# Performance work log

Measured on AMD Instinct MI355X. Metric: run time of the kernel, lower is better.

## Reference

```python
import jax, jax.numpy as jnp
import numpy as np

VOCAB = 32000


def setup_inputs() -> dict:
    key = jax.random.key(0)
    k1, k2, k3, k4, k5 = jax.random.split(key, 5)
    B, H, DEC_T, ATTN_LEN, D = 16, 12, 128, 512, 768
    return {
        "dec_output": jax.random.normal(k1, (B, DEC_T, D), dtype=jnp.float32),
        "final_output": jax.random.normal(k2, (B, DEC_T, VOCAB), dtype=jnp.float32),
        "attention_weights": jax.random.normal(k3, (B, H, DEC_T, ATTN_LEN), dtype=jnp.float32),
        "encoder_input": jax.random.randint(k4, (B, ATTN_LEN), 0, VOCAB, dtype=jnp.int32),
        "W_pg": jax.random.normal(k5, (D, 1), dtype=jnp.float32) / np.sqrt(D),
        "b_pg": jnp.zeros((1,), dtype=jnp.float32),
    }


def reference(dec_output, final_output, attention_weights, encoder_input, W_pg, b_pg):
    # p_gen: Dense(1) + sigmoid  -> [B, dec_t, 1]
    p_gen = jax.nn.sigmoid(dec_output @ W_pg + b_pg)

    vocab_dist = jax.nn.softmax(final_output, axis=-1)          # [B, dec_t, V]

    # mean_attention_heads=True: average over the heads axis
    attn_mean = jnp.mean(attention_weights, axis=1)              # [B, dec_t, attn_len]
    attn_dist = jax.nn.softmax(attn_mean, axis=-1)

    vocab_dists = p_gen * vocab_dist
    attn_dists = (1.0 - p_gen) * attn_dist

    dec_t = attn_dist.shape[1]

    # Per-example scatter-add of attention mass onto vocab ids.
    # For each batch b: proj[t, encoder_input[b, j]] += attn_dists[b, t, j]
    def scatter_one(ids, a):  # ids: [attn_len] int, a: [dec_t, attn_len]
        return jnp.zeros((dec_t, VOCAB), dtype=a.dtype).at[:, ids].add(a)

    attn_dists_projected = jax.vmap(scatter_one)(encoder_input, attn_dists)

    final_dists = attn_dists_projected + vocab_dists
    return jnp.log(final_dists)
```

## Files before the change

### kernel.cpp

```cpp
#include <hip/hip_runtime.h>
#include <math.h>

#define VOCAB 32000
#define NB 16
#define NH 12
#define DEC_T 128
#define ALEN 512
#define DD 768
#define NT 1024
#define NW 16
#define V4 8000
#define CHUNKS 8

__device__ inline float wave_sum(float v) {
#pragma unroll
  for (int o = 32; o > 0; o >>= 1) v += __shfl_down(v, o, 64);
  return v;
}
__device__ inline float wave_max(float v) {
#pragma unroll
  for (int o = 32; o > 0; o >>= 1) v = fmaxf(v, __shfl_down(v, o, 64));
  return v;
}

__global__ __launch_bounds__(NT, 4) void pg_kernel(
    const float* __restrict__ dec, const float* __restrict__ fo,
    const float* __restrict__ attnw, const int* __restrict__ ids,
    const float* __restrict__ Wpg, const float* __restrict__ bpg,
    float* __restrict__ out) {
  __shared__ float s_vocab[VOCAB];
  __shared__ float s_red[NW];
  __shared__ float s_res[8];

  const int bt = blockIdx.x;
  const int b = bt / DEC_T;
  const int t = bt - b * DEC_T;
  const int tid = threadIdx.x;
  const int lane = tid & 63;
  const int wid = tid >> 6;

  const float4* row4 = (const float4*)(fo + (size_t)bt * VOCAB);
  float4 r[CHUNKS];
#pragma unroll
  for (int c = 0; c < CHUNKS; ++c) {
    int idx = c * NT + tid;
    if (idx < V4) r[c] = row4[idx];
  }

  for (int i = tid; i < VOCAB; i += NT) s_vocab[i] = 0.f;

  float pp = 0.f;
  if (tid < DD) pp = dec[(size_t)bt * DD + tid] * Wpg[tid];
  pp = wave_sum(pp);
  if (lane == 0) s_red[wid] = pp;
  __syncthreads();
  if (tid == 0) {
    float acc = 0.f;
    for (int i = 0; i < NW; ++i) acc += s_red[i];
    s_res[0] = acc;
  }
  __syncthreads();
  const float pgen = 1.f / (1.f + __expf(-(s_res[0] + bpg[0])));

  float amean = 0.f;
  float av = -INFINITY;
  if (tid < ALEN) {
    const float* ap = attnw + ((size_t)b * NH * DEC_T + t) * ALEN + tid;
    float s = 0.f;
#pragma unroll
    for (int h = 0; h < NH; ++h) s += ap[(size_t)h * DEC_T * ALEN];
    amean = s * (1.f / NH);
    av = amean;
  }
  float am = wave_max(av);
  if (lane == 0) s_red[wid] = am;
  __syncthreads();
  if (tid == 0) {
    float acc = -INFINITY;
    for (int i = 0; i < NW; ++i) acc = fmaxf(acc, s_red[i]);
    s_res[1] = acc;
  }
  __syncthreads();
  const float amax = s_res[1];
  float ae = (tid < ALEN) ? __expf(amean - amax) : 0.f;
  float as = wave_sum(ae);
  if (lane == 0) s_red[wid] = as;
  __syncthreads();
  if (tid == 0) {
    float acc = 0.f;
    for (int i = 0; i < NW; ++i) acc += s_red[i];
    s_res[2] = acc;
  }
  __syncthreads();
  const float ainv = (1.f - pgen) / s_res[2];
  if (tid < ALEN) atomicAdd(&s_vocab[ids[b * ALEN + tid]], ae * ainv);

  float m = -INFINITY;
#pragma unroll
  for (int c = 0; c < CHUNKS; ++c) {
    int idx = c * NT + tid;
    if (idx < V4)
      m = fmaxf(m, fmaxf(fmaxf(r[c].x, r[c].y), fmaxf(r[c].z, r[c].w)));
  }
  m = wave_max(m);
  if (lane == 0) s_red[wid] = m;
  __syncthreads();
  if (tid == 0) {
    float acc = -INFINITY;
    for (int i = 0; i < NW; ++i) acc = fmaxf(acc, s_red[i]);
    s_res[3] = acc;
  }
  __syncthreads();
  const float fm = s_res[3];

  float zs = 0.f;
#pragma unroll
  for (int c = 0; c < CHUNKS; ++c) {
    int idx = c * NT + tid;
    if (idx < V4)
      zs += __expf(r[c].x - fm) + __expf(r[c].y - fm) +
            __expf(r[c].z - fm) + __expf(r[c].w - fm);
  }
  zs = wave_sum(zs);
  if (lane == 0) s_red[wid] = zs;
  __syncthreads();
  if (tid == 0) {
    float acc = 0.f;
    for (int i = 0; i < NW; ++i) acc += s_red[i];
    s_res[4] = acc;
  }
  __syncthreads();
  const float Z = s_res[4];
  const float invZ = 1.f / Z;
  const float C = __logf(pgen) - fm - __logf(Z);

  float4* out4 = (float4*)(out + (size_t)bt * VOCAB);
#pragma unroll
  for (int c = 0; c < CHUNKS; ++c) {
    int idx = c * NT + tid;
    if (idx < V4) {
      const int v = idx * 4;
      const float4 x = r[c];
      const float s0 = s_vocab[v + 0];
      const float s1 = s_vocab[v + 1];
      const float s2 = s_vocab[v + 2];
      const float s3 = s_vocab[v + 3];
      float4 o;
      o.x = (s0 == 0.f) ? (x.x + C) : __logf(pgen * __expf(x.x - fm) * invZ + s0);
      o.y = (s1 == 0.f) ? (x.y + C) : __logf(pgen * __expf(x.y - fm) * invZ + s1);
      o.z = (s2 == 0.f) ? (x.z + C) : __logf(pgen * __expf(x.z - fm) * invZ + s2);
      o.w = (s3 == 0.f) ? (x.w + C) : __logf(pgen * __expf(x.w - fm) * invZ + s3);
      out4[idx] = o;
    }
  }
}

extern "C" void kernel_launch(void* const* d_in, const int* in_sizes, int n_in,
                              void* d_out, int out_size, void* d_ws, size_t ws_size,
                              hipStream_t stream) {
  (void)in_sizes; (void)n_in; (void)out_size; (void)d_ws; (void)ws_size;
  const float* dec   = (const float*)d_in[0];
  const float* fo    = (const float*)d_in[1];
  const float* attnw = (const float*)d_in[2];
  const int*   ids   = (const int*)  d_in[3];
  const float* Wpg   = (const float*)d_in[4];
  const float* bpg   = (const float*)d_in[5];
  float* out = (float*)d_out;

  pg_kernel<<<NB * DEC_T, NT, 0, stream>>>(dec, fo, attnw, ids, Wpg, bpg, out);
}
```

Baseline: 481.3 us.

## Replace dense vocab LDS array with hash table plus bitmap, halve block size

Result: slower. 513.9 us (+6.8%).

```diff
diff --git a/kernel.cpp b/kernel.cpp
--- a/kernel.cpp
+++ b/kernel.cpp
@@ -7,10 +7,14 @@
 #define DEC_T 128
 #define ALEN 512
 #define DD 768
-#define NT 1024
-#define NW 16
+#define NT 512
+#define NW 8
 #define V4 8000
-#define CHUNKS 8
+#define CHUNKS 16
+#define HSZ 1024
+#define BMW 1000
+
+typedef float f4 __attribute__((ext_vector_type(4)));
 
 __device__ inline float wave_sum(float v) {
 #pragma unroll
@@ -28,9 +32,11 @@
     const float* __restrict__ attnw, const int* __restrict__ ids,
     const float* __restrict__ Wpg, const float* __restrict__ bpg,
     float* __restrict__ out) {
-  __shared__ float s_vocab[VOCAB];
-  __shared__ float s_red[NW];
-  __shared__ float s_res[8];
+  __shared__ int      h_key[HSZ];
+  __shared__ float    h_val[HSZ];
+  __shared__ unsigned bm[BMW];
+  __shared__ float    s_red[NW];
+  __shared__ float    s_res[8];
 
   const int bt = blockIdx.x;
   const int b = bt / DEC_T;
@@ -39,18 +45,27 @@
   const int lane = tid & 63;
   const int wid = tid >> 6;
 
-  const float4* row4 = (const float4*)(fo + (size_t)bt * VOCAB);
-  float4 r[CHUNKS];
+  const f4* row4 = (const f4*)(fo + (size_t)bt * VOCAB);
+  f4 r[CHUNKS];
 #pragma unroll
   for (int c = 0; c < CHUNKS; ++c) {
     int idx = c * NT + tid;
-    if (idx < V4) r[c] = row4[idx];
+    if (idx < V4) {
+      r[c] = row4[idx];
+    } else {
+      f4 z = {0.f, 0.f, 0.f, 0.f};
+      r[c] = z;
+    }
   }
+#pragma unroll
+  for (int c = 0; c < CHUNKS; ++c) asm volatile("" : "+v"(r[c]));
 
-  for (int i = tid; i < VOCAB; i += NT) s_vocab[i] = 0.f;
+  for (int i = tid; i < HSZ; i += NT) { h_key[i] = -1; h_val[i] = 0.f; }
+  for (int i = tid; i < BMW; i += NT) bm[i] = 0u;
 
-  float pp = 0.f;
-  if (tid < DD) pp = dec[(size_t)bt * DD + tid] * Wpg[tid];
+  const float* drow = dec + (size_t)bt * DD;
+  float pp = drow[tid] * Wpg[tid];
+  if (tid < DD - NT) pp += drow[tid + NT] * Wpg[tid + NT];
   pp = wave_sum(pp);
   if (lane == 0) s_red[wid] = pp;
   __syncthreads();
@@ -62,17 +77,12 @@
   __syncthreads();
   const float pgen = 1.f / (1.f + __expf(-(s_res[0] + bpg[0])));
 
-  float amean = 0.f;
-  float av = -INFINITY;
-  if (tid < ALEN) {
-    const float* ap = attnw + ((size_t)b * NH * DEC_T + t) * ALEN + tid;
-    float s = 0.f;
+  const float* ap = attnw + ((size_t)b * NH * DEC_T + t) * ALEN + tid;
+  float s = 0.f;
 #pragma unroll
-    for (int h = 0; h < NH; ++h) s += ap[(size_t)h * DEC_T * ALEN];
-    amean = s * (1.f / NH);
-    av = amean;
-  }
-  float am = wave_max(av);
+  for (int h = 0; h < NH; ++h) s += ap[(size_t)h * DEC_T * ALEN];
+  const float amean = s * (1.f / NH);
+  float am = wave_max(amean);
   if (lane == 0) s_red[wid] = am;
   __syncthreads();
   if (tid == 0) {
@@ -81,8 +91,7 @@
     s_res[1] = acc;
   }
   __syncthreads();
-  const float amax = s_res[1];
-  float ae = (tid < ALEN) ? __expf(amean - amax) : 0.f;
+  const float ae = __expf(amean - s_res[1]);
   float as = wave_sum(ae);
   if (lane == 0) s_red[wid] = as;
   __syncthreads();
@@ -93,7 +102,18 @@
   }
   __syncthreads();
   const float ainv = (1.f - pgen) / s_res[2];
-  if (tid < ALEN) atomicAdd(&s_vocab[ids[b * ALEN + tid]], ae * ainv);
+
+  {
+    const int id = ids[b * ALEN + tid];
+    const float contrib = ae * ainv;
+    atomicOr(&bm[id >> 5], 1u << (id & 31));
+    unsigned h = ((unsigned)id * 2654435761u) >> 22;
+    while (true) {
+      int old = atomicCAS(&h_key[h], -1, id);
+      if (old == -1 || old == id) { atomicAdd(&h_val[h], contrib); break; }
+      h = (h + 1) & (HSZ - 1);
+    }
+  }
 
   float m = -INFINITY;
 #pragma unroll
@@ -130,29 +150,35 @@
     s_res[4] = acc;
   }
   __syncthreads();
-  const float Z = s_res[4];
-  const float invZ = 1.f / Z;
-  const float C = __logf(pgen) - fm - __logf(Z);
+  const float P = pgen / s_res[4];
+  const float C = __logf(P) - fm;
 
-  float4* out4 = (float4*)(out + (size_t)bt * VOCAB);
+#define FIXUP(comp, k)                                                     \
+  if (bits & (1u << (k))) {                                                \
+    int v = idx * 4 + (k);                                                 \
+    unsigned h = ((unsigned)v * 2654435761u) >> 22;                        \
+    while (h_key[h] != v) h = (h + 1) & (HSZ - 1);                         \
+    o.comp = __logf(P * __expf(x.comp - fm) + h_val[h]);                   \
+  }
+
+  f4* out4 = (f4*)(out + (size_t)bt * VOCAB);
 #pragma unroll
   for (int c = 0; c < CHUNKS; ++c) {
     int idx = c * NT + tid;
     if (idx < V4) {
-      const int v = idx * 4;
-      const float4 x = r[c];
-      const float s0 = s_vocab[v + 0];
-      const float s1 = s_vocab[v + 1];
-      const float s2 = s_vocab[v + 2];
-      const float s3 = s_vocab[v + 3];
-      float4 o;
-      o.x = (s0 == 0.f) ? (x.x + C) : __logf(pgen * __expf(x.x - fm) * invZ + s0);
-      o.y = (s1 == 0.f) ? (x.y + C) : __logf(pgen * __expf(x.y - fm) * invZ + s1);
-      o.z = (s2 == 0.f) ? (x.z + C) : __logf(pgen * __expf(x.z - fm) * invZ + s2);
-      o.w = (s3 == 0.f) ? (x.w + C) : __logf(pgen * __expf(x.w - fm) * invZ + s3);
+      const f4 x = r[c];
+      f4 o = x + C;
+      unsigned bits = (bm[idx >> 3] >> ((idx & 7) * 4)) & 0xFu;
+      if (bits) {
+        FIXUP(x, 0)
+        FIXUP(y, 1)
+        FIXUP(z, 2)
+        FIXUP(w, 3)
+      }
       out4[idx] = o;
     }
   }
+#undef FIXUP
 }
 
 extern "C" void kernel_launch(void* const* d_in, const int* in_sizes, int n_in,
```
